# Performance work log

Hardware: AMD Instinct MI355X
Metric: run time of the kernel (lower is better)

The kernel has to match this reference:

```python
import jax, jax.numpy as jnp
import numpy as np

N_NODES = 50000
N_EDGES = 500000
D = 128  # node/edge feature dim


def setup_inputs() -> dict:
    key = jax.random.key(0)
    k1, k2, k3, k4, k5 = jax.random.split(key, 5)
    x_node = jax.random.normal(k1, (N_NODES, D), dtype=jnp.float32)
    x_edge = jax.random.normal(k2, (N_EDGES, D), dtype=jnp.float32)
    edge_index = jax.random.randint(k3, (N_EDGES, 2), 0, N_NODES, dtype=jnp.int64)
    # MLP params: Linear(3D -> D) -> ReLU -> Linear(D -> D)
    W1 = jax.random.normal(k4, (3 * D, D), dtype=jnp.float32) * (1.0 / np.sqrt(3 * D))
    b1 = jnp.zeros((D,), dtype=jnp.float32)
    W2 = jax.random.normal(k5, (D, D), dtype=jnp.float32) * (1.0 / np.sqrt(D))
    b2 = jnp.zeros((D,), dtype=jnp.float32)
    return {"x_node": x_node, "x_edge": x_edge, "edge_index": edge_index,
            "W1": W1, "b1": b1, "W2": W2, "b2": b2}


def reference(x_node, x_edge, edge_index, W1, b1, W2, b2):
    # gather node features at both endpoints of each edge
    v0 = x_node[edge_index[:, 0]]          # [E, D]
    v1 = x_node[edge_index[:, 1]]          # [E, D]
    x_new = jnp.concatenate([v0, v1, x_edge], axis=1)  # [E, 3D]
    h = jax.nn.relu(x_new @ W1 + b1)       # [E, D]
    x_edge_new = h @ W2 + b2               # [E, D]
    return x_edge_new
```

## Files before the change

kernel.cpp:

```cpp
#include <hip/hip_runtime.h>
#include <stdint.h>

#define D 128
#define MT 64

typedef short short8 __attribute__((ext_vector_type(8)));
typedef float f32x16 __attribute__((ext_vector_type(16)));

__device__ __forceinline__ unsigned short f2bf(float f) {
    union { float f; uint32_t u; } v;
    v.f = f;
    uint32_t u = v.u;
    uint32_t r = (u + 0x7fffu + ((u >> 16) & 1u)) >> 16;
    return (unsigned short)r;
}

__global__ void pack_weights_kernel(const float* __restrict__ W1,
                                    const float* __restrict__ W2,
                                    unsigned short* __restrict__ W1p,
                                    unsigned short* __restrict__ W2p) {
    int t = blockIdx.x * 256 + threadIdx.x;
    if (t < 6144) {
        int kt = t >> 8, nt = (t >> 6) & 3, lane = t & 63;
        int n = nt * 32 + (lane & 31);
        int kb = kt * 16 + (lane >> 5) * 8;
        unsigned short* dst = W1p + t * 8;
        #pragma unroll
        for (int j = 0; j < 8; ++j) dst[j] = f2bf(W1[(kb + j) * D + n]);
    } else if (t < 8192) {
        int u = t - 6144;
        int kt = u >> 8, nt = (u >> 6) & 3, lane = u & 63;
        int n = nt * 32 + (lane & 31);
        int kb = kt * 16 + (lane >> 5) * 8;
        unsigned short* dst = W2p + u * 8;
        #pragma unroll
        for (int j = 0; j < 8; ++j) dst[j] = f2bf(W2[(kb + j) * D + n]);
    }
}

__global__ __launch_bounds__(256, 3) void edge_mlp_kernel(
    const float* __restrict__ x_node,
    const float* __restrict__ x_edge,
    const int* __restrict__ eidx,
    const unsigned short* __restrict__ W1p,
    const unsigned short* __restrict__ W2p,
    const float* __restrict__ b1,
    const float* __restrict__ b2,
    float* __restrict__ out,
    int E) {
    __shared__ unsigned short lds[MT * 392];
    unsigned short* Hs = lds;

    const int t = threadIdx.x;
    const int r0 = blockIdx.x * MT;

    {
        const int lane32 = t & 31;
        const int rsub = t >> 5;
        #pragma unroll
        for (int rb = 0; rb < 8; ++rb) {
            int row = rb * 8 + rsub;
            int rg = r0 + row;
            int rgc = rg < E ? rg : E - 1;
            int e0 = eidx[2 * rgc];
            int e1 = eidx[2 * rgc + 1];
            float4 v0 = ((const float4*)(x_node + (size_t)e0 * D))[lane32];
            float4 v1 = ((const float4*)(x_node + (size_t)e1 * D))[lane32];
            float4 v2 = ((const float4*)(x_edge + (size_t)rgc * D))[lane32];
            unsigned short* base = &lds[row * 392 + lane32 * 4];
            ushort4 p;
            p.x = f2bf(v0.x); p.y = f2bf(v0.y); p.z = f2bf(v0.z); p.w = f2bf(v0.w);
            *(ushort4*)(base) = p;
            p.x = f2bf(v1.x); p.y = f2bf(v1.y); p.z = f2bf(v1.z); p.w = f2bf(v1.w);
            *(ushort4*)(base + 128) = p;
            p.x = f2bf(v2.x); p.y = f2bf(v2.y); p.z = f2bf(v2.z); p.w = f2bf(v2.w);
            *(ushort4*)(base + 256) = p;
        }
    }
    __syncthreads();

    const int w = t >> 6;
    const int lane = t & 63;
    const int lrow = lane & 31;
    const int khalf = (lane >> 5) * 8;
    const int n = w * 32 + lrow;
    const int rbump = (lane >> 5) * 4;

    f32x16 acc0, acc1;
    #pragma unroll
    for (int i = 0; i < 16; ++i) { acc0[i] = 0.f; acc1[i] = 0.f; }

    for (int kt = 0; kt < 24; ++kt) {
        short8 a0 = *(const short8*)&lds[lrow * 392 + kt * 16 + khalf];
        short8 a1 = *(const short8*)&lds[(lrow + 32) * 392 + kt * 16 + khalf];
        short8 b  = *(const short8*)(W1p + ((kt * 4 + w) * 64 + lane) * 8);
        acc0 = __builtin_amdgcn_mfma_f32_32x32x16_bf16(a0, b, acc0, 0, 0, 0);
        acc1 = __builtin_amdgcn_mfma_f32_32x32x16_bf16(a1, b, acc1, 0, 0, 0);
    }
    __syncthreads();

    {
        float b1v = b1[n];
        #pragma unroll
        for (int r = 0; r < 16; ++r) {
            int rr = (r & 3) + 8 * (r >> 2) + rbump;
            float h0 = fmaxf(acc0[r] + b1v, 0.f);
            float h1 = fmaxf(acc1[r] + b1v, 0.f);
            Hs[rr * 136 + n] = f2bf(h0);
            Hs[(rr + 32) * 136 + n] = f2bf(h1);
        }
    }
    __syncthreads();

    f32x16 c0, c1;
    #pragma unroll
    for (int i = 0; i < 16; ++i) { c0[i] = 0.f; c1[i] = 0.f; }

    #pragma unroll
    for (int kt = 0; kt < 8; ++kt) {
        short8 a0 = *(const short8*)&Hs[lrow * 136 + kt * 16 + khalf];
        short8 a1 = *(const short8*)&Hs[(lrow + 32) * 136 + kt * 16 + khalf];
        short8 b  = *(const short8*)(W2p + ((kt * 4 + w) * 64 + lane) * 8);
        c0 = __builtin_amdgcn_mfma_f32_32x32x16_bf16(a0, b, c0, 0, 0, 0);
        c1 = __builtin_amdgcn_mfma_f32_32x32x16_bf16(a1, b, c1, 0, 0, 0);
    }

    {
        float b2v = b2[n];
        #pragma unroll
        for (int r = 0; r < 16; ++r) {
            int rr = (r & 3) + 8 * (r >> 2) + rbump;
            int rg = r0 + rr;
            if (rg < E) out[(size_t)rg * D + n] = c0[r] + b2v;
            if (rg + 32 < E) out[(size_t)(rg + 32) * D + n] = c1[r] + b2v;
        }
    }
}

extern "C" void kernel_launch(void* const* d_in, const int* in_sizes, int n_in,
                              void* d_out, int out_size, void* d_ws, size_t ws_size,
                              hipStream_t stream) {
    const float* x_node = (const float*)d_in[0];
    const float* x_edge = (const float*)d_in[1];
    const int*   eidx   = (const int*)d_in[2];
    const float* W1     = (const float*)d_in[3];
    const float* b1     = (const float*)d_in[4];
    const float* W2     = (const float*)d_in[5];
    const float* b2     = (const float*)d_in[6];
    float* out = (float*)d_out;

    const int E = in_sizes[1] / D;

    unsigned short* W1p = (unsigned short*)d_ws;
    unsigned short* W2p = W1p + 6144 * 8;

    pack_weights_kernel<<<32, 256, 0, stream>>>(W1, W2, W1p, W2p);

    int nblk = (E + MT - 1) / MT;
    edge_mlp_kernel<<<nblk, 256, 0, stream>>>(x_node, x_edge, eidx, W1p, W2p, b1, b2, out, E);
}
```

Measured before the change: 533.3 us.

## Split 64-row tile across 8 waves with one MFMA accumulator each

Raises the block from 256 to 512 threads so each of 8 waves computes one 32x32 output tile (a row half and column block) instead of two. The gather loop is rebalanced across the larger block. The goal is lower per-wave register pressure and more latency hiding for the memory-bound gather through more resident waves. In exchange, each wave now loads its own B fragment for a single MFMA, so W1/W2 fragment loads per block double and A-reuse per B load is lost.

```diff
diff --git a/kernel.cpp b/kernel.cpp
--- a/kernel.cpp
+++ b/kernel.cpp
@@ -38,7 +38,7 @@
     }
 }
 
-__global__ __launch_bounds__(256, 3) void edge_mlp_kernel(
+__global__ __launch_bounds__(512, 6) void edge_mlp_kernel(
     const float* __restrict__ x_node,
     const float* __restrict__ x_edge,
     const int* __restrict__ eidx,
@@ -58,8 +58,8 @@
         const int lane32 = t & 31;
         const int rsub = t >> 5;
         #pragma unroll
-        for (int rb = 0; rb < 8; ++rb) {
-            int row = rb * 8 + rsub;
+        for (int rb = 0; rb < 4; ++rb) {
+            int row = rb * 16 + rsub;
             int rg = r0 + row;
             int rgc = rg < E ? rg : E - 1;
             int e0 = eidx[2 * rgc];
@@ -80,22 +80,23 @@
     __syncthreads();
 
     const int w = t >> 6;
+    const int cb = w & 3;
+    const int rt = w >> 2;
     const int lane = t & 63;
     const int lrow = lane & 31;
     const int khalf = (lane >> 5) * 8;
-    const int n = w * 32 + lrow;
+    const int n = cb * 32 + lrow;
     const int rbump = (lane >> 5) * 4;
+    const int arow = rt * 32 + lrow;
 
-    f32x16 acc0, acc1;
+    f32x16 acc;
     #pragma unroll
-    for (int i = 0; i < 16; ++i) { acc0[i] = 0.f; acc1[i] = 0.f; }
+    for (int i = 0; i < 16; ++i) acc[i] = 0.f;
 
     for (int kt = 0; kt < 24; ++kt) {
-        short8 a0 = *(const short8*)&lds[lrow * 392 + kt * 16 + khalf];
-        short8 a1 = *(const short8*)&lds[(lrow + 32) * 392 + kt * 16 + khalf];
-        short8 b  = *(const short8*)(W1p + ((kt * 4 + w) * 64 + lane) * 8);
-        acc0 = __builtin_amdgcn_mfma_f32_32x32x16_bf16(a0, b, acc0, 0, 0, 0);
-        acc1 = __builtin_amdgcn_mfma_f32_32x32x16_bf16(a1, b, acc1, 0, 0, 0);
+        short8 a = *(const short8*)&lds[arow * 392 + kt * 16 + khalf];
+        short8 b = *(const short8*)(W1p + ((kt * 4 + cb) * 64 + lane) * 8);
+        acc = __builtin_amdgcn_mfma_f32_32x32x16_bf16(a, b, acc, 0, 0, 0);
     }
     __syncthreads();
 
@@ -103,36 +104,30 @@
         float b1v = b1[n];
         #pragma unroll
         for (int r = 0; r < 16; ++r) {
-            int rr = (r & 3) + 8 * (r >> 2) + rbump;
-            float h0 = fmaxf(acc0[r] + b1v, 0.f);
-            float h1 = fmaxf(acc1[r] + b1v, 0.f);
-            Hs[rr * 136 + n] = f2bf(h0);
-            Hs[(rr + 32) * 136 + n] = f2bf(h1);
+            int rr = rt * 32 + (r & 3) + 8 * (r >> 2) + rbump;
+            Hs[rr * 136 + n] = f2bf(fmaxf(acc[r] + b1v, 0.f));
         }
     }
     __syncthreads();
 
-    f32x16 c0, c1;
+    f32x16 c;
     #pragma unroll
-    for (int i = 0; i < 16; ++i) { c0[i] = 0.f; c1[i] = 0.f; }
+    for (int i = 0; i < 16; ++i) c[i] = 0.f;
 
     #pragma unroll
     for (int kt = 0; kt < 8; ++kt) {
-        short8 a0 = *(const short8*)&Hs[lrow * 136 + kt * 16 + khalf];
-        short8 a1 = *(const short8*)&Hs[(lrow + 32) * 136 + kt * 16 + khalf];
-        short8 b  = *(const short8*)(W2p + ((kt * 4 + w) * 64 + lane) * 8);
-        c0 = __builtin_amdgcn_mfma_f32_32x32x16_bf16(a0, b, c0, 0, 0, 0);
-        c1 = __builtin_amdgcn_mfma_f32_32x32x16_bf16(a1, b, c1, 0, 0, 0);
+        short8 a = *(const short8*)&Hs[arow * 136 + kt * 16 + khalf];
+        short8 b = *(const short8*)(W2p + ((kt * 4 + cb) * 64 + lane) * 8);
+        c = __builtin_amdgcn_mfma_f32_32x32x16_bf16(a, b, c, 0, 0, 0);
     }
 
     {
         float b2v = b2[n];
         #pragma unroll
         for (int r = 0; r < 16; ++r) {
-            int rr = (r & 3) + 8 * (r >> 2) + rbump;
+            int rr = rt * 32 + (r & 3) + 8 * (r >> 2) + rbump;
             int rg = r0 + rr;
-            if (rg < E) out[(size_t)rg * D + n] = c0[r] + b2v;
-            if (rg + 32 < E) out[(size_t)(rg + 32) * D + n] = c1[r] + b2v;
+            if (rg < E) out[(size_t)rg * D + n] = c[r] + b2v;
         }
     }
 }
@@ -157,5 +152,5 @@
     pack_weights_kernel<<<32, 256, 0, stream>>>(W1, W2, W1p, W2p);
 
     int nblk = (E + MT - 1) / MT;
-    edge_mlp_kernel<<<nblk, 256, 0, stream>>>(x_node, x_edge, eidx, W1p, W2p, b1, b2, out, E);
+    edge_mlp_kernel<<<nblk, 512, 0, stream>>>(x_node, x_edge, eidx, W1p, W2p, b1, b2, out, E);
 }
```

New measurement: 520.5 us. 1.02x faster.
